# Kernel optimization log

Measured on AMD Instinct MI355X. Metric: run time of the kernel, lower is better.

Reference implementation:

```python
import jax, jax.numpy as jnp
import numpy as np

# DeepSeek-V3-style gate config
TOP_K = 8
N_EXPERTS = 256
N_GROUP = 8
TOPK_GROUP = 4
ROUTED_SCALING = 2.5
EPS = 1e-20


def setup_inputs() -> dict:
    key = jax.random.key(0)
    k1, k2, k3 = jax.random.split(key, 3)
    S, H = 16384, 7168
    hidden_states = jax.random.normal(k1, (S, H), dtype=jnp.float32)
    weight = jax.random.normal(k2, (N_EXPERTS, H), dtype=jnp.float32) * 0.02
    e_score_correction_bias = jax.random.normal(k3, (N_EXPERTS,), dtype=jnp.float32) * 0.1
    return {"hidden_states": hidden_states, "weight": weight,
            "e_score_correction_bias": e_score_correction_bias}


def reference(hidden_states, weight, e_score_correction_bias):
    S = hidden_states.shape[0]
    group_size = N_EXPERTS // N_GROUP  # 32

    # gating GEMM: [S, E]
    router_logits = jnp.einsum('sh,eh->se', hidden_states, weight)
    # scoring_func == 'sigmoid'
    scores = jax.nn.sigmoid(router_logits)
    scores_for_choice = scores + e_score_correction_bias[None, :]

    # group scores: sum of top-2 biased scores within each group -> [S, G]
    grouped = scores_for_choice.reshape(S, N_GROUP, group_size)
    top2_vals, _ = jax.lax.top_k(grouped, 2)
    group_scores = top2_vals.sum(axis=-1)

    # select top `TOPK_GROUP` groups, build group mask
    _, group_idx = jax.lax.top_k(group_scores, TOPK_GROUP)  # [S, topk_group]
    group_mask = jnp.zeros((S, N_GROUP), dtype=scores.dtype)
    group_mask = group_mask.at[jnp.arange(S)[:, None], group_idx].set(1.0)
    score_mask = jnp.repeat(group_mask, group_size, axis=-1)  # [S, E]

    # masked top-k over experts; weights gathered from UNBIASED scores
    tmp_scores = jnp.where(score_mask > 0, scores_for_choice, 0.0)
    _, topk_idx = jax.lax.top_k(tmp_scores, TOP_K)  # [S, top_k]
    topk_weight = jnp.take_along_axis(scores, topk_idx, axis=1)

    # renormalize (top_k > 1 and norm_topk_prob) then scale (noaux_tc)
    denom = topk_weight.sum(axis=-1, keepdims=True) + EPS
    topk_weight = topk_weight / denom * ROUTED_SCALING
    return topk_weight, topk_idx
```

## Files before the change

kernel.cpp:

```cpp
#include <hip/hip_runtime.h>
#include <math.h>

#define H_DIM 7168
#define N_EXP 256
#define N_GRP 8
#define G_SZ  32
#define TOPK_G 4
#define TOPK   8
#define BM 128
#define BK 32
#define S_TOK 16384
#define NTILES (H_DIM / BK)
#define NSPLIT 4
#define NQ     (NTILES / NSPLIT)
#define ITILES 2
#define NINT   (NQ / ITILES)
#define TILE_W_BYTES 32768
#define TILE_A_BYTES 16384

#define SA_SCALE 256.0f
#define SW_SCALE 4096.0f
#define DESCALE  (1.0f / 1048576.0f)

__device__ __align__(256) char g_wimg[(size_t)NTILES * TILE_W_BYTES];
__device__ __align__(256) float g_part[NSPLIT * (size_t)S_TOK * N_EXP];

typedef __attribute__((ext_vector_type(8))) _Float16 f16x8;
typedef __attribute__((ext_vector_type(4))) float f32x4;
typedef __attribute__((ext_vector_type(4))) unsigned short u16x4;
typedef __attribute__((ext_vector_type(8))) unsigned short u16x8;

__device__ inline void split2h(float x, unsigned short& h, unsigned short& l) {
    _Float16 hf = (_Float16)x;
    _Float16 lf = (_Float16)(x - (float)hf);
    h = __builtin_bit_cast(unsigned short, hf);
    l = __builtin_bit_cast(unsigned short, lf);
}

__global__ __launch_bounds__(256)
void convert_w_kernel(const float* __restrict__ W) {
    int idx  = blockIdx.x * 256 + threadIdx.x;
    int e    = idx / (H_DIM / 8);
    int koct = idx - e * (H_DIM / 8);
    int k0   = koct * 8;
    int t    = k0 >> 5;
    int o    = (k0 >> 3) & 3;
    int lane = (e & 15) | (o << 4);
    int w    = e >> 5;
    int nj   = (e >> 4) & 1;
    const float* src = W + (size_t)e * H_DIM + k0;
    unsigned short h[8], l[8];
    #pragma unroll
    for (int j = 0; j < 8; ++j)
        split2h(src[j] * SW_SCALE, h[j], l[j]);
    char* base = g_wimg + (size_t)t * TILE_W_BYTES + (w << 12) + (lane << 4);
    *(u16x8*)(base + nj * 1024)       = u16x8{h[0],h[1],h[2],h[3],h[4],h[5],h[6],h[7]};
    *(u16x8*)(base + (2 + nj) * 1024) = u16x8{l[0],l[1],l[2],l[3],l[4],l[5],l[6],l[7]};
}

__global__ __launch_bounds__(512, 2)
void moe_gemm_quarter(const float* __restrict__ A)
{
    __shared__ __align__(128) char smem[2 * ITILES * TILE_A_BYTES];

    const int tid   = threadIdx.x;
    const int lane  = tid & 63;
    const int wave  = tid >> 6;
    const int b     = blockIdx.x;
    const int kq    = b & 3;
    const int brow  = (b >> 2) * BM;

    const int fr   = lane & 15;
    const int fkb  = (lane >> 4) << 4;
    const int fswz = ((fr << 6) + fkb) ^ ((fr & 7) << 4);

    const int ar   = tid >> 3;
    const int akq  = tid & 7;
    const int aswz = ((ar << 6) + (akq << 3)) ^ ((ar & 7) << 4);
    const float4* Ag4 = reinterpret_cast<const float4*>(
        A + (size_t)(brow + ar) * H_DIM + kq * (H_DIM / NSPLIT)) + akq;
    const size_t ROW64 = (size_t)64 * (H_DIM / 4);

    f32x4 acc[8][2] = {};

    auto writeA2 = [&](const float4& v0, const float4& v1, char* ab) {
        unsigned short h0[4], l0[4], h1[4], l1[4];
        split2h(v0.x * SA_SCALE, h0[0], l0[0]); split2h(v0.y * SA_SCALE, h0[1], l0[1]);
        split2h(v0.z * SA_SCALE, h0[2], l0[2]); split2h(v0.w * SA_SCALE, h0[3], l0[3]);
        split2h(v1.x * SA_SCALE, h1[0], l1[0]); split2h(v1.y * SA_SCALE, h1[1], l1[1]);
        split2h(v1.z * SA_SCALE, h1[2], l1[2]); split2h(v1.w * SA_SCALE, h1[3], l1[3]);
        *(u16x4*)(ab + aswz)         = u16x4{h0[0], h0[1], h0[2], h0[3]};
        *(u16x4*)(ab + 4096 + aswz)  = u16x4{h1[0], h1[1], h1[2], h1[3]};
        *(u16x4*)(ab + 8192 + aswz)  = u16x4{l0[0], l0[1], l0[2], l0[3]};
        *(u16x4*)(ab + 12288 + aswz) = u16x4{l1[0], l1[1], l1[2], l1[3]};
    };

    const char* wsrc = g_wimg + (size_t)(kq * NQ) * TILE_W_BYTES
                       + (wave << 12) + (lane << 4);

    auto doTile = [&](int t, const char* ab) {
        const char* p = wsrc + (size_t)t * TILE_W_BYTES;
        f16x8 bh0 = *(const f16x8*)(p + 0);
        f16x8 bh1 = *(const f16x8*)(p + 1024);
        f16x8 bl0 = *(const f16x8*)(p + 2048);
        f16x8 bl1 = *(const f16x8*)(p + 3072);
        #pragma unroll
        for (int mb = 0; mb < 2; ++mb) {
            f16x8 ah[4];
            #pragma unroll
            for (int m = 0; m < 4; ++m)
                ah[m] = *(const f16x8*)(ab + (mb * 4 + m) * 1024 + fswz);
            __builtin_amdgcn_s_setprio(1);
            #pragma unroll
            for (int m = 0; m < 4; ++m)
                acc[mb*4+m][0] = __builtin_amdgcn_mfma_f32_16x16x32_f16(ah[m], bh0, acc[mb*4+m][0], 0, 0, 0);
            #pragma unroll
            for (int m = 0; m < 4; ++m)
                acc[mb*4+m][1] = __builtin_amdgcn_mfma_f32_16x16x32_f16(ah[m], bh1, acc[mb*4+m][1], 0, 0, 0);
            #pragma unroll
            for (int m = 0; m < 4; ++m)
                acc[mb*4+m][0] = __builtin_amdgcn_mfma_f32_16x16x32_f16(ah[m], bl0, acc[mb*4+m][0], 0, 0, 0);
            #pragma unroll
            for (int m = 0; m < 4; ++m)
                acc[mb*4+m][1] = __builtin_amdgcn_mfma_f32_16x16x32_f16(ah[m], bl1, acc[mb*4+m][1], 0, 0, 0);
            __builtin_amdgcn_s_setprio(0);
            f16x8 al[4];
            #pragma unroll
            for (int m = 0; m < 4; ++m)
                al[m] = *(const f16x8*)(ab + 8192 + (mb * 4 + m) * 1024 + fswz);
            __builtin_amdgcn_s_setprio(1);
            #pragma unroll
            for (int m = 0; m < 4; ++m)
                acc[mb*4+m][0] = __builtin_amdgcn_mfma_f32_16x16x32_f16(al[m], bh0, acc[mb*4+m][0], 0, 0, 0);
            #pragma unroll
            for (int m = 0; m < 4; ++m)
                acc[mb*4+m][1] = __builtin_amdgcn_mfma_f32_16x16x32_f16(al[m], bh1, acc[mb*4+m][1], 0, 0, 0);
            __builtin_amdgcn_s_setprio(0);
        }
    };

    {
        float4 a00 = Ag4[0],      a01 = Ag4[ROW64];
        float4 a10 = Ag4[8],      a11 = Ag4[ROW64 + 8];
        writeA2(a00, a01, smem);
        writeA2(a10, a11, smem + TILE_A_BYTES);
        asm volatile("s_waitcnt lgkmcnt(0)" ::: "memory");
        __builtin_amdgcn_s_barrier();
    }

    #pragma unroll 1
    for (int i = 0; i < NINT; ++i) {
        char* cur = smem + (i & 1) * (ITILES * TILE_A_BYTES);
        char* nxt = smem + ((i + 1) & 1) * (ITILES * TILE_A_BYTES);
        const bool havenext = (i + 1 < NINT);
        const int ib = (havenext ? i + 1 : i) * ITILES;

        doTile(i * ITILES, cur);
        if (havenext) {
            float4 a00 = Ag4[(size_t)(ib + 0) * 8];
            float4 a01 = Ag4[ROW64 + (size_t)(ib + 0) * 8];
            float4 a10 = Ag4[(size_t)(ib + 1) * 8];
            float4 a11 = Ag4[ROW64 + (size_t)(ib + 1) * 8];
            writeA2(a00, a01, nxt);
            writeA2(a10, a11, nxt + TILE_A_BYTES);
        }
        doTile(i * ITILES + 1, cur + TILE_A_BYTES);
        asm volatile("s_waitcnt lgkmcnt(0)" ::: "memory");
        __builtin_amdgcn_s_barrier();
    }

    float* pb = g_part + ((size_t)kq * S_TOK + brow) * N_EXP;
    #pragma unroll
    for (int mi = 0; mi < 8; ++mi)
        #pragma unroll
        for (int nj = 0; nj < 2; ++nj)
            #pragma unroll
            for (int q = 0; q < 4; ++q) {
                int row = mi * 16 + ((lane >> 4) << 2) + q;
                int col = (wave << 5) + (nj << 4) + (lane & 15);
                pb[row * N_EXP + col] = acc[mi][nj][q];
            }
}

__global__ __launch_bounds__(256)
void gate_kernel(const float* __restrict__ bias, float* __restrict__ out, int S)
{
    const int lane = threadIdx.x & 63;
    const int row  = (blockIdx.x * 256 + threadIdx.x) >> 6;

    const float4 p0 = *(const float4*)(g_part + (size_t)row * N_EXP + lane * 4);
    const float4 p1 = *(const float4*)(g_part + ((size_t)S_TOK + row) * N_EXP + lane * 4);
    const float4 p2 = *(const float4*)(g_part + (2 * (size_t)S_TOK + row) * N_EXP + lane * 4);
    const float4 p3 = *(const float4*)(g_part + (3 * (size_t)S_TOK + row) * N_EXP + lane * 4);
    const float4 b4 = *(const float4*)(bias + lane * 4);

    float s[4], v[4];
    float m1 = -1e30f, m2 = -1e30f;
    {
        const float* q0 = (const float*)&p0;
        const float* q1 = (const float*)&p1;
        const float* q2 = (const float*)&p2;
        const float* q3 = (const float*)&p3;
        const float* qb = (const float*)&b4;
        #pragma unroll
        for (int j = 0; j < 4; ++j) {
            float x = (((q0[j] + q1[j]) + q2[j]) + q3[j]) * DESCALE;
            s[j] = 1.0f / (1.0f + expf(-x));
            float sb = s[j] + qb[j];
            v[j] = sb;
            if (sb > m1) { m2 = m1; m1 = sb; } else if (sb > m2) { m2 = sb; }
        }
    }
    #pragma unroll
    for (int d = 1; d < 8; d <<= 1) {
        float om1 = __shfl_xor(m1, d), om2 = __shfl_xor(m2, d);
        float hi = fmaxf(m1, om1), lo = fminf(m1, om1);
        m1 = hi;
        m2 = fmaxf(lo, fmaxf(m2, om2));
    }
    float gs = m1 + m2;
    float gsv[8];
    #pragma unroll
    for (int g = 0; g < 8; ++g) gsv[g] = __shfl(gs, g << 3);

    unsigned gmask = 0;
    #pragma unroll
    for (int t = 0; t < TOPK_G; ++t) {
        float best = -1e30f; int bg = 0;
        #pragma unroll
        for (int g = 0; g < 8; ++g) {
            bool avail = !((gmask >> g) & 1);
            if (avail && gsv[g] > best) { best = gsv[g]; bg = g; }
        }
        gmask |= 1u << bg;
    }

    const bool sel = (gmask >> (lane >> 3)) & 1;
    #pragma unroll
    for (int j = 0; j < 4; ++j) v[j] = sel ? v[j] : 0.0f;

    float wv[TOPK]; int wi[TOPK]; float wsum = 0.0f;
    #pragma unroll
    for (int t = 0; t < TOPK; ++t) {
        float bv = v[0]; int bj = 0;
        #pragma unroll
        for (int j = 1; j < 4; ++j)
            if (v[j] > bv) { bv = v[j]; bj = j; }
        int bidx = (lane << 2) | bj;
        #pragma unroll
        for (int d = 32; d >= 1; d >>= 1) {
            float ov = __shfl_xor(bv, d);
            int   oi = __shfl_xor(bidx, d);
            if (ov > bv || (ov == bv && oi < bidx)) { bv = ov; bidx = oi; }
        }
        int ol = bidx >> 2, oj = bidx & 3;
        float sl = s[0];
        if (oj == 1) sl = s[1]; else if (oj == 2) sl = s[2]; else if (oj == 3) sl = s[3];
        float sv = __shfl(sl, ol);
        wv[t] = sv; wi[t] = bidx; wsum += sv;
        if (lane == ol) {
            if (oj == 0) v[0] = -1e30f; else if (oj == 1) v[1] = -1e30f;
            else if (oj == 2) v[2] = -1e30f; else v[3] = -1e30f;
        }
    }

    if (lane == 0) {
        float scale = 2.5f / (wsum + 1e-20f);
        #pragma unroll
        for (int t = 0; t < TOPK; ++t) {
            out[(size_t)row * TOPK + t] = wv[t] * scale;
            out[(size_t)S * TOPK + (size_t)row * TOPK + t] = (float)wi[t];
        }
    }
}

extern "C" void kernel_launch(void* const* d_in, const int* in_sizes, int n_in,
                              void* d_out, int out_size, void* d_ws, size_t ws_size,
                              hipStream_t stream) {
    const float* A    = (const float*)d_in[0];
    const float* W    = (const float*)d_in[1];
    const float* bias = (const float*)d_in[2];
    float* out = (float*)d_out;
    const int S = in_sizes[0] / H_DIM;

    convert_w_kernel<<<dim3(N_EXP * (H_DIM / 8) / 256), 256, 0, stream>>>(W);
    moe_gemm_quarter<<<dim3(NSPLIT * S / BM), 512, 0, stream>>>(A);
    gate_kernel<<<dim3(S / 4), 256, 0, stream>>>(bias, out, S);
}
```

Measured before the change: 208.7 us.

## Retile GEMM waves to 64x64 blocks to balance A and W fragment reuse

Changes the per-wave output tile from 128 rows by 32 experts to 64 rows by 64 experts, arranged as a 2x4 wave grid. The weight image layout is rewritten so that each wave reads four hi/lo B fragments from a contiguous 8KB region. Each wave now loads fewer A fragments from LDS per tile and more B fragments from global memory, trading LDS read traffic for more global/L2 weight reads. The accumulator count per wave is unchanged.

Result: slower. 234.0 us (+12.1%).

```diff
diff --git a/kernel.cpp b/kernel.cpp
--- a/kernel.cpp
+++ b/kernel.cpp
@@ -46,16 +46,16 @@
     int t    = k0 >> 5;
     int o    = (k0 >> 3) & 3;
     int lane = (e & 15) | (o << 4);
-    int w    = e >> 5;
-    int nj   = (e >> 4) & 1;
+    int eq   = e >> 6;
+    int nj   = (e >> 4) & 3;
     const float* src = W + (size_t)e * H_DIM + k0;
     unsigned short h[8], l[8];
     #pragma unroll
     for (int j = 0; j < 8; ++j)
         split2h(src[j] * SW_SCALE, h[j], l[j]);
-    char* base = g_wimg + (size_t)t * TILE_W_BYTES + (w << 12) + (lane << 4);
-    *(u16x8*)(base + nj * 1024)       = u16x8{h[0],h[1],h[2],h[3],h[4],h[5],h[6],h[7]};
-    *(u16x8*)(base + (2 + nj) * 1024) = u16x8{l[0],l[1],l[2],l[3],l[4],l[5],l[6],l[7]};
+    char* base = g_wimg + (size_t)t * TILE_W_BYTES + (eq << 13) + (nj << 10) + (lane << 4);
+    *(u16x8*)(base)        = u16x8{h[0],h[1],h[2],h[3],h[4],h[5],h[6],h[7]};
+    *(u16x8*)(base + 4096) = u16x8{l[0],l[1],l[2],l[3],l[4],l[5],l[6],l[7]};
 }
 
 __global__ __launch_bounds__(512, 2)
@@ -66,13 +66,16 @@
     const int tid   = threadIdx.x;
     const int lane  = tid & 63;
     const int wave  = tid >> 6;
+    const int mh    = wave >> 2;
+    const int eq    = wave & 3;
     const int b     = blockIdx.x;
     const int kq    = b & 3;
     const int brow  = (b >> 2) * BM;
 
-    const int fr   = lane & 15;
-    const int fkb  = (lane >> 4) << 4;
-    const int fswz = ((fr << 6) + fkb) ^ ((fr & 7) << 4);
+    const int fr    = lane & 15;
+    const int fkb   = (lane >> 4) << 4;
+    const int fswz  = ((fr << 6) + fkb) ^ ((fr & 7) << 4);
+    const int abase = (mh << 12) + fswz;
 
     const int ar   = tid >> 3;
     const int akq  = tid & 7;
@@ -81,7 +84,7 @@
         A + (size_t)(brow + ar) * H_DIM + kq * (H_DIM / NSPLIT)) + akq;
     const size_t ROW64 = (size_t)64 * (H_DIM / 4);
 
-    f32x4 acc[8][2] = {};
+    f32x4 acc[4][4] = {};
 
     auto writeA2 = [&](const float4& v0, const float4& v1, char* ab) {
         unsigned short h0[4], l0[4], h1[4], l1[4];
@@ -96,47 +99,43 @@
     };
 
     const char* wsrc = g_wimg + (size_t)(kq * NQ) * TILE_W_BYTES
-                       + (wave << 12) + (lane << 4);
+                       + (eq << 13) + (lane << 4);
 
     auto doTile = [&](int t, const char* ab) {
         const char* p = wsrc + (size_t)t * TILE_W_BYTES;
-        f16x8 bh0 = *(const f16x8*)(p + 0);
-        f16x8 bh1 = *(const f16x8*)(p + 1024);
-        f16x8 bl0 = *(const f16x8*)(p + 2048);
-        f16x8 bl1 = *(const f16x8*)(p + 3072);
-        #pragma unroll
-        for (int mb = 0; mb < 2; ++mb) {
-            f16x8 ah[4];
+        f16x8 bh[4], bl[4];
+        #pragma unroll
+        for (int nj = 0; nj < 4; ++nj) {
+            bh[nj] = *(const f16x8*)(p + (nj << 10));
+            bl[nj] = *(const f16x8*)(p + 4096 + (nj << 10));
+        }
+        f16x8 ah[4];
+        #pragma unroll
+        for (int m = 0; m < 4; ++m)
+            ah[m] = *(const f16x8*)(ab + abase + m * 1024);
+        __builtin_amdgcn_s_setprio(1);
+        #pragma unroll
+        for (int nj = 0; nj < 4; ++nj)
             #pragma unroll
             for (int m = 0; m < 4; ++m)
-                ah[m] = *(const f16x8*)(ab + (mb * 4 + m) * 1024 + fswz);
-            __builtin_amdgcn_s_setprio(1);
+                acc[m][nj] = __builtin_amdgcn_mfma_f32_16x16x32_f16(ah[m], bh[nj], acc[m][nj], 0, 0, 0);
+        #pragma unroll
+        for (int nj = 0; nj < 4; ++nj)
             #pragma unroll
             for (int m = 0; m < 4; ++m)
-                acc[mb*4+m][0] = __builtin_amdgcn_mfma_f32_16x16x32_f16(ah[m], bh0, acc[mb*4+m][0], 0, 0, 0);
+                acc[m][nj] = __builtin_amdgcn_mfma_f32_16x16x32_f16(ah[m], bl[nj], acc[m][nj], 0, 0, 0);
+        __builtin_amdgcn_s_setprio(0);
+        f16x8 al[4];
+        #pragma unroll
+        for (int m = 0; m < 4; ++m)
+            al[m] = *(const f16x8*)(ab + 8192 + abase + m * 1024);
+        __builtin_amdgcn_s_setprio(1);
+        #pragma unroll
+        for (int nj = 0; nj < 4; ++nj)
             #pragma unroll
             for (int m = 0; m < 4; ++m)
-                acc[mb*4+m][1] = __builtin_amdgcn_mfma_f32_16x16x32_f16(ah[m], bh1, acc[mb*4+m][1], 0, 0, 0);
-            #pragma unroll
-            for (int m = 0; m < 4; ++m)
-                acc[mb*4+m][0] = __builtin_amdgcn_mfma_f32_16x16x32_f16(ah[m], bl0, acc[mb*4+m][0], 0, 0, 0);
-            #pragma unroll
-            for (int m = 0; m < 4; ++m)
-                acc[mb*4+m][1] = __builtin_amdgcn_mfma_f32_16x16x32_f16(ah[m], bl1, acc[mb*4+m][1], 0, 0, 0);
-            __builtin_amdgcn_s_setprio(0);
-            f16x8 al[4];
-            #pragma unroll
-            for (int m = 0; m < 4; ++m)
-                al[m] = *(const f16x8*)(ab + 8192 + (mb * 4 + m) * 1024 + fswz);
-            __builtin_amdgcn_s_setprio(1);
-            #pragma unroll
-            for (int m = 0; m < 4; ++m)
-                acc[mb*4+m][0] = __builtin_amdgcn_mfma_f32_16x16x32_f16(al[m], bh0, acc[mb*4+m][0], 0, 0, 0);
-            #pragma unroll
-            for (int m = 0; m < 4; ++m)
-                acc[mb*4+m][1] = __builtin_amdgcn_mfma_f32_16x16x32_f16(al[m], bh1, acc[mb*4+m][1], 0, 0, 0);
-            __builtin_amdgcn_s_setprio(0);
-        }
+                acc[m][nj] = __builtin_amdgcn_mfma_f32_16x16x32_f16(al[m], bh[nj], acc[m][nj], 0, 0, 0);
+        __builtin_amdgcn_s_setprio(0);
     };
 
     {
@@ -171,14 +170,14 @@
 
     float* pb = g_part + ((size_t)kq * S_TOK + brow) * N_EXP;
     #pragma unroll
-    for (int mi = 0; mi < 8; ++mi)
-        #pragma unroll
-        for (int nj = 0; nj < 2; ++nj)
+    for (int m = 0; m < 4; ++m)
+        #pragma unroll
+        for (int nj = 0; nj < 4; ++nj)
             #pragma unroll
             for (int q = 0; q < 4; ++q) {
-                int row = mi * 16 + ((lane >> 4) << 2) + q;
-                int col = (wave << 5) + (nj << 4) + (lane & 15);
-                pb[row * N_EXP + col] = acc[mi][nj][q];
+                int row = (mh << 6) + m * 16 + ((lane >> 4) << 2) + q;
+                int col = (eq << 6) + nj * 16 + (lane & 15);
+                pb[row * N_EXP + col] = acc[m][nj][q];
             }
 }
 
```
